# Optimization experiments

Hardware: AMD Instinct MI355X
Metric: run time of the kernel (lower is better)

## Reference

```python
import jax, jax.numpy as jnp
import numpy as np

B, H, W, C = 4, 64, 64, 256
CQK = C // 8  # squeeze_times = 8


def setup_inputs() -> dict:
    key = jax.random.key(0)
    ks = jax.random.split(key, 7)
    s = 0.02
    return {
        "x": jax.random.normal(ks[0], (B, H, W, C), dtype=jnp.float32),
        "Wq": jax.random.normal(ks[1], (C, CQK), dtype=jnp.float32) * s,
        "bq": jnp.zeros((CQK,), dtype=jnp.float32),
        "Wk": jax.random.normal(ks[2], (C, CQK), dtype=jnp.float32) * s,
        "bk": jnp.zeros((CQK,), dtype=jnp.float32),
        "Wv": jax.random.normal(ks[3], (C, C), dtype=jnp.float32) * s,
        "bv": jnp.zeros((C,), dtype=jnp.float32),
        "gamma": jnp.zeros((), dtype=jnp.float32) + 0.5,  # nonzero so residual path is exercised
    }


def reference(x, Wq, bq, Wk, bk, Wv, bv, gamma):
    b, h, w, c = x.shape
    n = h * w
    # 1x1 convs == per-pixel dense layers
    q = x @ Wq + bq                       # (B,H,W,CQK)
    k = x @ Wk + bk                       # (B,H,W,CQK)
    v = x @ Wv + bv                       # (B,H,W,C)
    pq = q.reshape(b, n, -1)              # (B,N,CQK)
    pk = k.reshape(b, n, -1)              # (B,N,CQK)
    pv = v.reshape(b, n, -1)              # (B,N,C)
    # energy[b,i,j] = <q_i, k_j>, unscaled (as in original)
    energy = jnp.einsum('bid,bjd->bij', pq, pk)   # (B,N,N)
    attention = jax.nn.softmax(energy, axis=-1)   # softmax over last axis
    # out = proj_value (B,C,N) @ attention^T -> out[b,c,i] = sum_j v[b,j,c]*att[b,i,j]
    out = jnp.einsum('bjc,bij->bic', pv, attention)  # (B,N,C)
    out = out.reshape(b, h, w, c)
    return out * gamma + x, attention
```

## Files before the change

kernel.cpp:

```cpp
#include <hip/hip_runtime.h>

typedef __bf16 bf16_t;
typedef bf16_t bf16x8 __attribute__((ext_vector_type(8)));
typedef float f32x4 __attribute__((ext_vector_type(4)));

#define MFMA16(a, b, c) __builtin_amdgcn_mfma_f32_16x16x32_bf16(a, b, c, 0, 0, 0)

static __device__ __forceinline__ unsigned short f2bf(float f) {
  unsigned int u = __builtin_bit_cast(unsigned int, f);
  unsigned int r = (u + 0x7fffu + ((u >> 16) & 1u)) >> 16;
  return (unsigned short)r;
}

__global__ void prep_kernel(const float* __restrict__ x, const float* __restrict__ Wq,
                            const float* __restrict__ Wk, const float* __restrict__ Wv,
                            unsigned short* __restrict__ xb, unsigned short* __restrict__ Wt) {
  int tid = blockIdx.x * 256 + threadIdx.x;
  int stride = gridDim.x * 256;
  const float4* x4 = (const float4*)x;
  ushort4* xb4 = (ushort4*)xb;
  for (int i = tid; i < (4 * 4096 * 256) / 4; i += stride) {
    float4 v = x4[i];
    ushort4 o;
    o.x = f2bf(v.x); o.y = f2bf(v.y); o.z = f2bf(v.z); o.w = f2bf(v.w);
    xb4[i] = o;
  }
  for (int i = tid; i < 320 * 256; i += stride) {
    int n = i >> 8, k = i & 255;
    float v = (n < 32) ? Wq[k * 32 + n] : (n < 64) ? Wk[k * 32 + (n - 32)] : Wv[k * 256 + (n - 64)];
    Wt[i] = f2bf(v);
  }
}

__global__ __launch_bounds__(256) void qkv_kernel(
    const unsigned short* __restrict__ xb, const unsigned short* __restrict__ Wt,
    const float* __restrict__ bq, const float* __restrict__ bk, const float* __restrict__ bv,
    unsigned short* __restrict__ Qb, unsigned short* __restrict__ Kb,
    unsigned short* __restrict__ Vt) {
  __shared__ unsigned short wbuf[320 * 40];
  const int t = threadIdx.x;
  const int w = t >> 6, l = t & 63;
  const int lc = l & 15, lg = l >> 4;
  const int arow = blockIdx.x * 64 + w * 16 + lc;

  f32x4 acc[20];
#pragma unroll
  for (int i = 0; i < 20; i++) acc[i] = (f32x4){0.f, 0.f, 0.f, 0.f};

  for (int kk = 0; kk < 256; kk += 32) {
    __syncthreads();
#pragma unroll
    for (int i = 0; i < 5; i++) {
      int u = t + i * 256;
      int n = u >> 2, q = u & 3;
      *reinterpret_cast<bf16x8*>(&wbuf[n * 40 + q * 8]) =
          *reinterpret_cast<const bf16x8*>(&Wt[n * 256 + kk + q * 8]);
    }
    __syncthreads();
    bf16x8 af = *reinterpret_cast<const bf16x8*>(&xb[arow * 256 + kk + lg * 8]);
#pragma unroll
    for (int nt = 0; nt < 20; nt++) {
      bf16x8 bf = *reinterpret_cast<const bf16x8*>(&wbuf[(nt * 16 + lc) * 40 + lg * 8]);
      acc[nt] = MFMA16(af, bf, acc[nt]);
    }
  }
  const int orow = blockIdx.x * 64 + w * 16 + lg * 4;
#pragma unroll
  for (int nt = 0; nt < 20; nt++) {
    int co = nt * 16 + lc;
#pragma unroll
    for (int r = 0; r < 4; r++) {
      int R = orow + r;
      float v = acc[nt][r];
      if (co < 32) {
        Qb[R * 32 + co] = f2bf(v + bq[co]);
      } else if (co < 64) {
        Kb[R * 32 + (co - 32)] = f2bf(v + bk[co - 32]);
      } else {
        int c = co - 64;
        int bb = R >> 12, j = R & 4095;
        Vt[(((size_t)(bb * 128 + (j >> 5))) * 256 + c) * 32 + (j & 31)] = f2bf(v + bv[c]);
      }
    }
  }
}

__global__ __launch_bounds__(256) void attn_kernel(
    const unsigned short* __restrict__ Qb, const unsigned short* __restrict__ Kb,
    const unsigned short* __restrict__ Vt, const float* __restrict__ x,
    const float* __restrict__ gptr, float* __restrict__ out, float* __restrict__ att) {
  __shared__ unsigned short vbuf[2][256 * 40];
  __shared__ unsigned short pbuf[4][16 * 40];

  const int t = threadIdx.x;
  const int w = t >> 6, l = t & 63;
  const int lc = l & 15, lg = l >> 4;
  const int b = blockIdx.x >> 6;
  const int r0 = (blockIdx.x & 63) * 64 + w * 16;

  const unsigned short* Kbase = Kb + (size_t)b * 4096 * 32;
  const unsigned short* Vbase = Vt + (size_t)b * 128 * 8192;
  float* attb = att + (size_t)b * 4096 * 4096;

  auto loadK = [&](int ct) {
    return *reinterpret_cast<const bf16x8*>(&Kbase[(ct * 16 + lc) * 32 + lg * 8]);
  };

  bf16x8 aq = *reinterpret_cast<const bf16x8*>(&Qb[((size_t)b * 4096 + r0 + lc) * 32 + lg * 8]);
  const f32x4 zero = {0.f, 0.f, 0.f, 0.f};

  float s[4] = {0.f, 0.f, 0.f, 0.f};
  bf16x8 k0 = loadK(0), k1 = loadK(1), k2 = loadK(2), k3 = loadK(3);
  for (int ct = 0; ct < 256; ct += 4) {
    f32x4 d0 = MFMA16(aq, k0, zero); k0 = loadK(ct + 4);
    f32x4 d1 = MFMA16(aq, k1, zero); k1 = loadK(ct + 5);
    f32x4 d2 = MFMA16(aq, k2, zero); k2 = loadK(ct + 6);
    f32x4 d3 = MFMA16(aq, k3, zero); k3 = loadK(ct + 7);
#pragma unroll
    for (int r = 0; r < 4; r++)
      s[r] += __expf(d0[r] - 8.f) + __expf(d1[r] - 8.f) + __expf(d2[r] - 8.f) +
              __expf(d3[r] - 8.f);
  }
#pragma unroll
  for (int off = 1; off < 16; off <<= 1) {
#pragma unroll
    for (int r = 0; r < 4; r++) s[r] += __shfl_xor(s[r], off, 16);
  }
  float rinv[4];
#pragma unroll
  for (int r = 0; r < 4; r++) rinv[r] = 1.f / s[r];

  f32x4 acc[16];
#pragma unroll
  for (int i = 0; i < 16; i++) acc[i] = zero;

  auto stageLoad = [&](int jc, bf16x8* r) {
#pragma unroll
    for (int i = 0; i < 4; i++)
      r[i] = *reinterpret_cast<const bf16x8*>(&Vbase[(size_t)jc * 8192 + (t + i * 256) * 8]);
  };
  auto stageWrite = [&](unsigned short* buf, const bf16x8* r) {
#pragma unroll
    for (int i = 0; i < 4; i++) {
      int u = t + i * 256, c = u >> 2, q = u & 3;
      *reinterpret_cast<bf16x8*>(&buf[c * 40 + q * 8]) = r[i];
    }
  };

  bf16x8 vst[4];
  stageLoad(0, vst);
  stageWrite(vbuf[0], vst);
  bf16x8 kn0 = loadK(0), kn1 = loadK(1);
  __syncthreads();

  int cur = 0;
  for (int jc = 0; jc < 128; jc++) {
    bf16x8 kc0 = kn0, kc1 = kn1;
    bf16x8 vn[4];
    if (jc < 127) {
      stageLoad(jc + 1, vn);
      kn0 = loadK(jc * 2 + 2);
      kn1 = loadK(jc * 2 + 3);
    }
    f32x4 d0 = MFMA16(aq, kc0, zero);
    f32x4 d1 = MFMA16(aq, kc1, zero);
    unsigned short* pb = pbuf[w];
#pragma unroll
    for (int r = 0; r < 4; r++) {
      float p0 = __expf(d0[r] - 8.f) * rinv[r];
      float p1 = __expf(d1[r] - 8.f) * rinv[r];
      int grow = r0 + lg * 4 + r;
      size_t ai = (size_t)grow * 4096 + jc * 32;
      __builtin_nontemporal_store(p0, &attb[ai + lc]);
      __builtin_nontemporal_store(p1, &attb[ai + 16 + lc]);
      pb[(lg * 4 + r) * 40 + lc] = f2bf(p0);
      pb[(lg * 4 + r) * 40 + 16 + lc] = f2bf(p1);
    }
    bf16x8 pa = *reinterpret_cast<const bf16x8*>(&pb[lc * 40 + lg * 8]);
    const unsigned short* vb = vbuf[cur];
#pragma unroll
    for (int nt = 0; nt < 16; nt++) {
      bf16x8 bv = *reinterpret_cast<const bf16x8*>(&vb[(nt * 16 + lc) * 40 + lg * 8]);
      acc[nt] = MFMA16(pa, bv, acc[nt]);
    }
    if (jc < 127) stageWrite(vbuf[cur ^ 1], vn);
    __syncthreads();
    cur ^= 1;
  }

  const float gamma = *gptr;
#pragma unroll
  for (int nt = 0; nt < 16; nt++) {
#pragma unroll
    for (int r = 0; r < 4; r++) {
      size_t oi = ((size_t)(b * 4096 + r0 + lg * 4 + r)) * 256 + nt * 16 + lc;
      out[oi] = acc[nt][r] * gamma + x[oi];
    }
  }
}

extern "C" void kernel_launch(void* const* d_in, const int* in_sizes, int n_in, void* d_out,
                              int out_size, void* d_ws, size_t ws_size, hipStream_t stream) {
  const float* x = (const float*)d_in[0];
  const float* Wq = (const float*)d_in[1];
  const float* bq = (const float*)d_in[2];
  const float* Wk = (const float*)d_in[3];
  const float* bk = (const float*)d_in[4];
  const float* Wv = (const float*)d_in[5];
  const float* bv = (const float*)d_in[6];
  const float* gm = (const float*)d_in[7];
  float* out = (float*)d_out;
  float* att = out + (size_t)4 * 4096 * 256;

  char* ws = (char*)d_ws;
  unsigned short* xb = (unsigned short*)(ws);
  unsigned short* Wt = (unsigned short*)(ws + 8388608);
  unsigned short* Qb = (unsigned short*)(ws + 8552448);
  unsigned short* Kb = (unsigned short*)(ws + 9601024);
  unsigned short* Vt = (unsigned short*)(ws + 10649600);

  prep_kernel<<<2048, 256, 0, stream>>>(x, Wq, Wk, Wv, xb, Wt);
  qkv_kernel<<<256, 256, 0, stream>>>(xb, Wt, bq, bk, bv, Qb, Kb, Vt);
  attn_kernel<<<256, 256, 0, stream>>>(Qb, Kb, Vt, x, gm, out, att);
}
```

Before: 415.3 us.

## Split attention key range across two blocks and reduce partial outputs

The attention kernel now splits the key/value range in half across two blocks, doubling the grid to 512 blocks so more of the GPU's compute units are occupied. Partial P·V results go to a workspace and a new reduce kernel sums them, then applies gamma and the residual. The P·V product is reorganised so each wave covers all 64 rows and a quarter of the channels, sharing a block-wide P tile with an extra barrier. The qkv kernel also writes V transposed with 4-element vector stores. The cost is 32 MB of extra partial-output traffic and one more kernel launch.

```diff
diff --git a/kernel.cpp b/kernel.cpp
--- a/kernel.cpp
+++ b/kernel.cpp
@@ -68,35 +68,42 @@
 #pragma unroll
   for (int nt = 0; nt < 20; nt++) {
     int co = nt * 16 + lc;
-#pragma unroll
-    for (int r = 0; r < 4; r++) {
-      int R = orow + r;
-      float v = acc[nt][r];
-      if (co < 32) {
-        Qb[R * 32 + co] = f2bf(v + bq[co]);
-      } else if (co < 64) {
-        Kb[R * 32 + (co - 32)] = f2bf(v + bk[co - 32]);
-      } else {
-        int c = co - 64;
-        int bb = R >> 12, j = R & 4095;
-        Vt[(((size_t)(bb * 128 + (j >> 5))) * 256 + c) * 32 + (j & 31)] = f2bf(v + bv[c]);
+    if (co < 64) {
+#pragma unroll
+      for (int r = 0; r < 4; r++) {
+        int R = orow + r;
+        float v = acc[nt][r];
+        if (co < 32) Qb[R * 32 + co] = f2bf(v + bq[co]);
+        else Kb[R * 32 + (co - 32)] = f2bf(v + bk[co - 32]);
       }
+    } else {
+      int c = co - 64;
+      int bb = orow >> 12, j = orow & 4095;
+      ushort4 o;
+      o.x = f2bf(acc[nt][0] + bv[c]);
+      o.y = f2bf(acc[nt][1] + bv[c]);
+      o.z = f2bf(acc[nt][2] + bv[c]);
+      o.w = f2bf(acc[nt][3] + bv[c]);
+      *reinterpret_cast<ushort4*>(
+          &Vt[(((size_t)(bb * 128 + (j >> 5))) * 256 + c) * 32 + (j & 31)]) = o;
     }
   }
 }
 
 __global__ __launch_bounds__(256) void attn_kernel(
     const unsigned short* __restrict__ Qb, const unsigned short* __restrict__ Kb,
-    const unsigned short* __restrict__ Vt, const float* __restrict__ x,
-    const float* __restrict__ gptr, float* __restrict__ out, float* __restrict__ att) {
+    const unsigned short* __restrict__ Vt, float* __restrict__ pout,
+    float* __restrict__ att) {
   __shared__ unsigned short vbuf[2][256 * 40];
-  __shared__ unsigned short pbuf[4][16 * 40];
+  __shared__ unsigned short pbuf[2][64 * 40];
 
   const int t = threadIdx.x;
   const int w = t >> 6, l = t & 63;
   const int lc = l & 15, lg = l >> 4;
-  const int b = blockIdx.x >> 6;
-  const int r0 = (blockIdx.x & 63) * 64 + w * 16;
+  const int b = blockIdx.x >> 7;
+  const int rb = (blockIdx.x >> 1) & 63;
+  const int half = blockIdx.x & 1;
+  const int r0 = rb * 64;
 
   const unsigned short* Kbase = Kb + (size_t)b * 4096 * 32;
   const unsigned short* Vbase = Vt + (size_t)b * 128 * 8192;
@@ -106,7 +113,7 @@
     return *reinterpret_cast<const bf16x8*>(&Kbase[(ct * 16 + lc) * 32 + lg * 8]);
   };
 
-  bf16x8 aq = *reinterpret_cast<const bf16x8*>(&Qb[((size_t)b * 4096 + r0 + lc) * 32 + lg * 8]);
+  bf16x8 aq = *reinterpret_cast<const bf16x8*>(&Qb[((size_t)b * 4096 + r0 + w * 16 + lc) * 32 + lg * 8]);
   const f32x4 zero = {0.f, 0.f, 0.f, 0.f};
 
   float s[4] = {0.f, 0.f, 0.f, 0.f};
@@ -130,9 +137,11 @@
 #pragma unroll
   for (int r = 0; r < 4; r++) rinv[r] = 1.f / s[r];
 
-  f32x4 acc[16];
-#pragma unroll
-  for (int i = 0; i < 16; i++) acc[i] = zero;
+  f32x4 acc[4][4];
+#pragma unroll
+  for (int i = 0; i < 4; i++)
+#pragma unroll
+    for (int j = 0; j < 4; j++) acc[i][j] = zero;
 
   auto stageLoad = [&](int jc, bf16x8* r) {
 #pragma unroll
@@ -147,55 +156,82 @@
     }
   };
 
-  bf16x8 vst[4];
-  stageLoad(0, vst);
-  stageWrite(vbuf[0], vst);
-  bf16x8 kn0 = loadK(0), kn1 = loadK(1);
-  __syncthreads();
+  const int jc0 = half * 64;
+  bf16x8 vn[4];
+  stageLoad(jc0, vn);
+  bf16x8 kn0 = loadK(jc0 * 2), kn1 = loadK(jc0 * 2 + 1);
 
   int cur = 0;
-  for (int jc = 0; jc < 128; jc++) {
-    bf16x8 kc0 = kn0, kc1 = kn1;
-    bf16x8 vn[4];
-    if (jc < 127) {
+  for (int i = 0; i < 64; i++) {
+    const int jc = jc0 + i;
+    f32x4 d0 = MFMA16(aq, kn0, zero);
+    f32x4 d1 = MFMA16(aq, kn1, zero);
+    stageWrite(vbuf[cur], vn);
+    if (i < 63) {
       stageLoad(jc + 1, vn);
-      kn0 = loadK(jc * 2 + 2);
-      kn1 = loadK(jc * 2 + 3);
-    }
-    f32x4 d0 = MFMA16(aq, kc0, zero);
-    f32x4 d1 = MFMA16(aq, kc1, zero);
-    unsigned short* pb = pbuf[w];
+      kn0 = loadK((jc + 1) * 2);
+      kn1 = loadK((jc + 1) * 2 + 1);
+    }
+    unsigned short* pb = pbuf[cur];
 #pragma unroll
     for (int r = 0; r < 4; r++) {
       float p0 = __expf(d0[r] - 8.f) * rinv[r];
       float p1 = __expf(d1[r] - 8.f) * rinv[r];
-      int grow = r0 + lg * 4 + r;
+      int grow = r0 + w * 16 + lg * 4 + r;
       size_t ai = (size_t)grow * 4096 + jc * 32;
       __builtin_nontemporal_store(p0, &attb[ai + lc]);
       __builtin_nontemporal_store(p1, &attb[ai + 16 + lc]);
-      pb[(lg * 4 + r) * 40 + lc] = f2bf(p0);
-      pb[(lg * 4 + r) * 40 + 16 + lc] = f2bf(p1);
-    }
-    bf16x8 pa = *reinterpret_cast<const bf16x8*>(&pb[lc * 40 + lg * 8]);
+      pb[(w * 16 + lg * 4 + r) * 40 + lc] = f2bf(p0);
+      pb[(w * 16 + lg * 4 + r) * 40 + 16 + lc] = f2bf(p1);
+    }
+    __syncthreads();
     const unsigned short* vb = vbuf[cur];
-#pragma unroll
-    for (int nt = 0; nt < 16; nt++) {
-      bf16x8 bv = *reinterpret_cast<const bf16x8*>(&vb[(nt * 16 + lc) * 40 + lg * 8]);
-      acc[nt] = MFMA16(pa, bv, acc[nt]);
-    }
-    if (jc < 127) stageWrite(vbuf[cur ^ 1], vn);
-    __syncthreads();
+    const unsigned short* pbc = pbuf[cur];
+    bf16x8 pa[4];
+#pragma unroll
+    for (int rg = 0; rg < 4; rg++)
+      pa[rg] = *reinterpret_cast<const bf16x8*>(&pbc[(rg * 16 + lc) * 40 + lg * 8]);
+#pragma unroll
+    for (int ct = 0; ct < 4; ct++) {
+      bf16x8 bvv = *reinterpret_cast<const bf16x8*>(&vb[(w * 64 + ct * 16 + lc) * 40 + lg * 8]);
+#pragma unroll
+      for (int rg = 0; rg < 4; rg++) acc[rg][ct] = MFMA16(pa[rg], bvv, acc[rg][ct]);
+    }
     cur ^= 1;
   }
 
+  float* po = pout + (size_t)half * 4 * 4096 * 256;
+#pragma unroll
+  for (int rg = 0; rg < 4; rg++) {
+#pragma unroll
+    for (int ct = 0; ct < 4; ct++) {
+#pragma unroll
+      for (int r = 0; r < 4; r++) {
+        size_t oi = ((size_t)b * 4096 + r0 + rg * 16 + lg * 4 + r) * 256 + w * 64 + ct * 16 + lc;
+        po[oi] = acc[rg][ct][r];
+      }
+    }
+  }
+}
+
+__global__ void reduce_kernel(const float* __restrict__ p0, const float* __restrict__ p1,
+                              const float* __restrict__ x, const float* __restrict__ gptr,
+                              float* __restrict__ out) {
   const float gamma = *gptr;
-#pragma unroll
-  for (int nt = 0; nt < 16; nt++) {
-#pragma unroll
-    for (int r = 0; r < 4; r++) {
-      size_t oi = ((size_t)(b * 4096 + r0 + lg * 4 + r)) * 256 + nt * 16 + lc;
-      out[oi] = acc[nt][r] * gamma + x[oi];
-    }
+  int tid = blockIdx.x * 256 + threadIdx.x;
+  int stride = gridDim.x * 256;
+  const float4* a = (const float4*)p0;
+  const float4* c = (const float4*)p1;
+  const float4* xv = (const float4*)x;
+  float4* o = (float4*)out;
+  for (int i = tid; i < (4 * 4096 * 256) / 4; i += stride) {
+    float4 va = a[i], vc = c[i], vx = xv[i];
+    float4 r;
+    r.x = (va.x + vc.x) * gamma + vx.x;
+    r.y = (va.y + vc.y) * gamma + vx.y;
+    r.z = (va.z + vc.z) * gamma + vx.z;
+    r.w = (va.w + vc.w) * gamma + vx.w;
+    o[i] = r;
   }
 }
 
@@ -218,8 +254,10 @@
   unsigned short* Qb = (unsigned short*)(ws + 8552448);
   unsigned short* Kb = (unsigned short*)(ws + 9601024);
   unsigned short* Vt = (unsigned short*)(ws + 10649600);
+  float* pout = (float*)(ws + 19038208);
 
   prep_kernel<<<2048, 256, 0, stream>>>(x, Wq, Wk, Wv, xb, Wt);
   qkv_kernel<<<256, 256, 0, stream>>>(xb, Wt, bq, bk, bv, Qb, Kb, Vt);
-  attn_kernel<<<256, 256, 0, stream>>>(Qb, Kb, Vt, x, gm, out, att);
-}
+  attn_kernel<<<512, 256, 0, stream>>>(Qb, Kb, Vt, pout, att);
+  reduce_kernel<<<2048, 256, 0, stream>>>(pout, pout + (size_t)4 * 4096 * 256, x, gm, out);
+}
```

New measurement: 387.4 us. 6.7% less time.
